# Optimization experiments

Hardware: AMD Instinct MI355X
Metric: run time of the kernel (lower is better)

## Reference

```python
import jax, jax.numpy as jnp
import numpy as np

S, F, H, A, B = 11, 650, 1024, 47, 4096
NEG = -1e9  # stand-in for -inf in masked_fill; softmax weight becomes exactly 0 numerically


def _layernorm(x, g, b):
    m = x.mean(-1, keepdims=True)
    v = ((x - m) ** 2).mean(-1, keepdims=True)
    return (x - m) / jnp.sqrt(v + 1e-5) * g + b


def setup_inputs() -> dict:
    key = jax.random.key(0)
    ks = jax.random.split(key, 16)

    def lin(k, fan_in, fan_out):
        kw, kb = jax.random.split(k)
        s = 1.0 / np.sqrt(fan_in)
        W = jax.random.uniform(kw, (fan_in, fan_out), minval=-s, maxval=s, dtype=jnp.float32)
        b = jax.random.uniform(kb, (fan_out,), minval=-s, maxval=s, dtype=jnp.float32)
        return W, b

    obs = jax.random.normal(ks[0], (B, S, F), dtype=jnp.float32)
    action_mask = jax.random.randint(ks[1], (B, 2, A), 0, 2).astype(jnp.int32)
    action_mask = action_mask.at[:, :, :8].set(1)  # guarantee legal actions per row
    u = jax.random.uniform(ks[2], (B, 2, A), minval=1e-6, maxval=1.0)
    gumbel = -jnp.log(-jnp.log(u))

    W0, b0 = lin(ks[3], S * F, H)
    W1, b1 = lin(ks[4], H, H)
    W2, b2 = lin(ks[5], H, H)
    Wp, bp = lin(ks[6], H, 2 * A)
    Wv, bv = lin(ks[7], H, 1)
    ones = jnp.ones((H,), jnp.float32)
    zeros = jnp.zeros((H,), jnp.float32)
    return {
        'obs': obs, 'action_mask': action_mask, 'gumbel': gumbel,
        'W0': W0, 'b0': b0, 'g0': ones, 'be0': zeros,
        'W1': W1, 'b1': b1, 'g1': ones, 'be1': zeros,
        'W2': W2, 'b2': b2, 'g2': ones, 'be2': zeros,
        'Wp': Wp, 'bp': bp, 'Wv': Wv, 'bv': bv,
    }


def _forward(obs, action_mask, gumbel, W0, b0, g0, be0, W1, b1, g1, be1, W2, b2, g2, be2, Wp, bp, Wv, bv):
    x = obs.reshape(obs.shape[0], -1)
    x = jax.nn.relu(_layernorm(x @ W0 + b0, g0, be0))
    x = jax.nn.relu(_layernorm(x @ W1 + b1, g1, be1))
    x = jax.nn.relu(_layernorm(x @ W2 + b2, g2, be2))  # dropout = eval-mode identity
    policy_logits = (x @ Wp + bp).reshape(-1, 2, A)
    value = (x @ Wv + bv)[:, 0]

    bsz = policy_logits.shape[0]
    rows = jnp.arange(bsz)
    ar = jnp.arange(A)

    # head 1: masked categorical via Gumbel-max
    l1 = jnp.where(action_mask[:, 0, :] == 0, NEG, policy_logits[:, 0, :])
    a1 = jnp.argmax(l1 + gumbel[:, 0, :], axis=-1)
    logp1 = jax.nn.log_softmax(l1, axis=-1)[rows, a1]

    # vectorized mutual-exclusivity mask update (replaces per-batch Python loop)
    m2 = action_mask[:, 1, :]
    oh = ar[None, :] == a1[:, None]
    c_switch = (a1 >= 1) & (a1 <= 6)
    m2 = jnp.where(c_switch[:, None] & oh, 0, m2)
    c_tera = (a1 > 26) & (a1 <= 46)
    rng = (ar >= 27) & (ar < 47)
    m2 = jnp.where(c_tera[:, None] & rng[None, :], 0, m2)
    c_zero = a1 == 0
    col0 = (ar == 0)[None, :]
    m2 = jnp.where(c_zero[:, None] & col0, 0, m2)
    empty = (m2.sum(-1) == 0) & c_zero
    m2 = jnp.where(empty[:, None] & col0, 1, m2)

    l2 = jnp.where(m2 == 0, NEG, policy_logits[:, 1, :])
    a2 = jnp.argmax(l2 + gumbel[:, 1, :], axis=-1)
    logp2 = jax.nn.log_softmax(l2, axis=-1)[rows, a2]

    sampled_actions = jnp.stack([a1, a2], axis=-1)
    policy_log_probs = jnp.stack([logp1, logp2], axis=-1)
    return policy_logits, policy_log_probs, sampled_actions, value


def reference(obs, action_mask, gumbel, W0, b0, g0, be0, W1, b1, g1, be1, W2, b2, g2, be2, Wp, bp, Wv, bv):
    return _forward(obs, action_mask, gumbel, W0, b0, g0, be0, W1, b1, g1, be1, W2, b2, g2, be2, Wp, bp, Wv, bv)
```

## Files before the change

kernel.cpp:

```cpp
#include <hip/hip_runtime.h>
#include <math.h>

#define BATCH 4096
#define HDIM  1024
#define KDIM0 7150
#define KP0   7168
#define KT0   224
#define KTH   32
#define NACT  47
#define NA2   94
#define NEGC  -1000000000.0f

#define LP_OFF  385024
#define ACT_OFF 393216
#define VAL_OFF 401408

typedef _Float16 half8_t  __attribute__((ext_vector_type(8)));
typedef _Float16 half4_t  __attribute__((ext_vector_type(4)));
typedef float    float4_t __attribute__((ext_vector_type(4)));

#define GLOAD16(gp, lp) __builtin_amdgcn_global_load_lds( \
    (__attribute__((address_space(1))) void*)(gp), \
    (__attribute__((address_space(3))) void*)(lp), 16, 0, 0)


__global__ __launch_bounds__(256) void wconv_frag_kernel(
    const float* __restrict__ W, _Float16* __restrict__ Wh,
    _Float16* __restrict__ Wl, int K, int KT)
{
  __shared__ float T[64][65];
  const int k0 = blockIdx.x * 64, n0 = blockIdx.y * 64, t = threadIdx.x;
#pragma unroll
  for (int p = 0; p < 16; ++p) {
    const int idx = p * 256 + t;
    const int r = idx >> 6, c = idx & 63;
    T[r][c] = (k0 + r < K) ? W[(size_t)(k0 + r) * HDIM + n0 + c] : 0.f;
  }
  __syncthreads();
#pragma unroll
  for (int ss = 0; ss < 2; ++ss) {
    const int s    = ss * 256 + t;
    const int tile = s >> 6;
    const int ktl  = tile >> 2, ntl = tile & 3;
    const int lane = s & 63;
    const int quad = lane >> 4, nr = lane & 15;
    half8_t h, l;
#pragma unroll
    for (int j = 0; j < 8; ++j) {
      const float v = T[ktl * 32 + quad * 8 + j][ntl * 16 + nr];
      const _Float16 hh = (_Float16)v;
      h[j] = hh;
      l[j] = (_Float16)((v - (float)hh) * 4096.f);
    }
    const size_t o = ((size_t)((n0 / 16 + ntl) * KT + (k0 / 32 + ktl)) * 64 + lane) * 8;
    *(half8_t*)(Wh + o) = h;
    *(half8_t*)(Wl + o) = l;
  }
}

__global__ __launch_bounds__(256) void adecomp_frag_kernel(
    const float* __restrict__ A, _Float16* __restrict__ Ah,
    _Float16* __restrict__ Al)
{
  __shared__ float Xs[16][257];
  const int t  = threadIdx.x;
  const int mt = blockIdx.y;
  const int kb = blockIdx.x * 256;
  const int lr = t >> 4;
  const int lk = (t & 15) * 16;
  const float* src = A + (size_t)(mt * 16 + lr) * KDIM0 + kb + lk;
#pragma unroll
  for (int c = 0; c < 4; ++c) {
    const int kg = kb + lk + c * 4;
    float4 vv = make_float4(0.f, 0.f, 0.f, 0.f);
    if (kg + 3 < KDIM0) {
      vv = *(const float4*)(src + c * 4);
    } else {
      if (kg     < KDIM0) vv.x = src[c * 4];
      if (kg + 1 < KDIM0) vv.y = src[c * 4 + 1];
      if (kg + 2 < KDIM0) vv.z = src[c * 4 + 2];
      if (kg + 3 < KDIM0) vv.w = src[c * 4 + 3];
    }
    *(float4*)&Xs[lr][lk + c * 4] = vv;
  }
  __syncthreads();
#pragma unroll
  for (int ss = 0; ss < 2; ++ss) {
    const int s    = ss * 256 + t;
    const int ktl  = s >> 6;
    const int lane = s & 63;
    const int quad = lane >> 4, mr = lane & 15;
    half8_t h, l;
#pragma unroll
    for (int j = 0; j < 8; ++j) {
      const float v = Xs[mr][ktl * 32 + quad * 8 + j];
      const _Float16 hh = (_Float16)v;
      h[j] = hh;
      l[j] = (_Float16)((v - (float)hh) * 4096.f);
    }
    const size_t o = ((size_t)(mt * KT0 + blockIdx.x * 8 + ktl) * 64 + lane) * 8;
    *(half8_t*)(Ah + o) = h;
    *(half8_t*)(Al + o) = l;
  }
}

__global__ __launch_bounds__(512, 4) void gemm_frag2_kernel(
    const _Float16* __restrict__ Ah, const _Float16* __restrict__ Al,
    const _Float16* __restrict__ Wh, const _Float16* __restrict__ Wl,
    float* __restrict__ C, int KT, int ktsplit)
{
  __shared__ _Float16 As[2][2][8][512];
  __shared__ _Float16 Ws[2][2][8][512];
  const int t    = threadIdx.x;
  const int lane = t & 63;
  const int w    = t >> 6;
  const int nt0  = blockIdx.x * 8;
  const int mt0  = blockIdx.y * 8;
  const int ktb  = blockIdx.z * ktsplit;
  const int nit  = ktsplit >> 1;
  const int l15  = lane & 15, quad = lane >> 4;
  const int wmi  = (w >> 2) * 4;
  const int wni  = (w & 3) * 2;

  const _Float16* aS[2] = {
    Ah + (size_t)(mt0 + w) * KT * 512 + lane * 8,
    Al + (size_t)(mt0 + w) * KT * 512 + lane * 8 };
  const _Float16* wS[2] = {
    Wh + (size_t)(nt0 + w) * KT * 512 + lane * 8,
    Wl + (size_t)(nt0 + w) * KT * 512 + lane * 8 };

  float4_t acc[4][2], accx[4][2];
#pragma unroll
  for (int i = 0; i < 4; ++i)
#pragma unroll
    for (int j = 0; j < 2; ++j) {
      acc[i][j]  = (float4_t){0.f, 0.f, 0.f, 0.f};
      accx[i][j] = (float4_t){0.f, 0.f, 0.f, 0.f};
    }

  for (int it = 0; it < nit; ++it) {
    const size_t kb = (size_t)(ktb + it * 2) * 512;
#pragma unroll
    for (int k2 = 0; k2 < 2; ++k2)
#pragma unroll
      for (int pl = 0; pl < 2; ++pl) {
        GLOAD16(aS[pl] + kb + k2 * 512, &As[k2][pl][w][0]);
        GLOAD16(wS[pl] + kb + k2 * 512, &Ws[k2][pl][w][0]);
      }
    __syncthreads();
#pragma unroll
    for (int k2 = 0; k2 < 2; ++k2) {
      half8_t ah[4], al[4], wh[2], wl[2];
#pragma unroll
      for (int i = 0; i < 4; ++i) {
        ah[i] = *(const half8_t*)&As[k2][0][wmi + i][lane * 8];
        al[i] = *(const half8_t*)&As[k2][1][wmi + i][lane * 8];
      }
#pragma unroll
      for (int j = 0; j < 2; ++j) {
        wh[j] = *(const half8_t*)&Ws[k2][0][wni + j][lane * 8];
        wl[j] = *(const half8_t*)&Ws[k2][1][wni + j][lane * 8];
      }
#pragma unroll
      for (int i = 0; i < 4; ++i)
#pragma unroll
        for (int j = 0; j < 2; ++j) {
          acc[i][j]  = __builtin_amdgcn_mfma_f32_16x16x32_f16(ah[i], wh[j], acc[i][j], 0, 0, 0);
          accx[i][j] = __builtin_amdgcn_mfma_f32_16x16x32_f16(ah[i], wl[j], accx[i][j], 0, 0, 0);
          accx[i][j] = __builtin_amdgcn_mfma_f32_16x16x32_f16(al[i], wh[j], accx[i][j], 0, 0, 0);
        }
    }
    __syncthreads();
  }

  float* Cb = C + (size_t)blockIdx.z * ((size_t)BATCH * HDIM);
  const float sc = 1.0f / 4096.0f;
#pragma unroll
  for (int i = 0; i < 4; ++i) {
    const int row0 = (mt0 + wmi + i) * 16 + quad * 4;
#pragma unroll
    for (int j = 0; j < 2; ++j) {
      const int col = (nt0 + wni + j) * 16 + l15;
      float* cp = Cb + (size_t)row0 * HDIM + col;
#pragma unroll
      for (int r = 0; r < 4; ++r)
        cp[(size_t)r * HDIM] = acc[i][j][r] + accx[i][j][r] * sc;
    }
  }
}

__global__ __launch_bounds__(1024) void ln_relu_f16_frag_kernel(
    const float* __restrict__ x0, const float* __restrict__ x1,
    const float* __restrict__ bias,
    const float* __restrict__ g, const float* __restrict__ be,
    _Float16* __restrict__ oh, _Float16* __restrict__ ol)
{
  const int t = threadIdx.x;
  const int w = t >> 6, lane = t & 63;
  const int mt = blockIdx.x;
  const float* xr0 = x0 + (size_t)(mt * 16 + w) * HDIM;
  const float* xr1 = x1 + (size_t)(mt * 16 + w) * HDIM;

  float4 v[4];
  float s = 0.f;
#pragma unroll
  for (int c = 0; c < 4; ++c) {
    const int k = c * 256 + lane * 4;
    const float4 a = *(const float4*)(xr0 + k);
    const float4 b = *(const float4*)(xr1 + k);
    const float4 bb = *(const float4*)(bias + k);
    v[c].x = a.x + b.x + bb.x; v[c].y = a.y + b.y + bb.y;
    v[c].z = a.z + b.z + bb.z; v[c].w = a.w + b.w + bb.w;
    s += (v[c].x + v[c].y) + (v[c].z + v[c].w);
  }
#pragma unroll
  for (int o = 32; o; o >>= 1) s += __shfl_xor(s, o, 64);
  const float mean = s * (1.0f / HDIM);

  float s2 = 0.f;
#pragma unroll
  for (int c = 0; c < 4; ++c) {
    v[c].x -= mean; v[c].y -= mean; v[c].z -= mean; v[c].w -= mean;
    s2 += (v[c].x * v[c].x + v[c].y * v[c].y) + (v[c].z * v[c].z + v[c].w * v[c].w);
  }
#pragma unroll
  for (int o = 32; o; o >>= 1) s2 += __shfl_xor(s2, o, 64);
  const float inv = 1.0f / sqrtf(s2 * (1.0f / HDIM) + 1e-5f);

  const int kt_b  = lane >> 3;
  const int quad  = (lane >> 1) & 3;
  const int jb    = (lane & 1) * 4;
#pragma unroll
  for (int c = 0; c < 4; ++c) {
    const int k = c * 256 + lane * 4;
    const float4 gg = *(const float4*)(g + k);
    const float4 ee = *(const float4*)(be + k);
    float r0 = fmaxf(fmaf(v[c].x * inv, gg.x, ee.x), 0.f);
    float r1 = fmaxf(fmaf(v[c].y * inv, gg.y, ee.y), 0.f);
    float r2 = fmaxf(fmaf(v[c].z * inv, gg.z, ee.z), 0.f);
    float r3 = fmaxf(fmaf(v[c].w * inv, gg.w, ee.w), 0.f);
    const _Float16 h0 = (_Float16)r0, h1 = (_Float16)r1, h2 = (_Float16)r2, h3 = (_Float16)r3;
    const half4_t hv = {h0, h1, h2, h3};
    const half4_t lv = {(_Float16)((r0 - (float)h0) * 4096.f),
                        (_Float16)((r1 - (float)h1) * 4096.f),
                        (_Float16)((r2 - (float)h2) * 4096.f),
                        (_Float16)((r3 - (float)h3) * 4096.f)};
    const int kt = c * 8 + kt_b;
    const size_t o = ((size_t)(mt * KTH + kt) * 64 + quad * 16 + w) * 8 + jb;
    *(half4_t*)(oh + o) = hv;
    *(half4_t*)(ol + o) = lv;
  }
}

__global__ __launch_bounds__(256) void pack_wcat_kernel(
    const float* __restrict__ Wp, const float* __restrict__ Wv,
    float* __restrict__ Wc)
{
  const int i = blockIdx.x * 256 + threadIdx.x;
  const int k = i / 96, c = i % 96;
  float v = 0.f;
  if (c < 94)       v = Wp[(size_t)k * 94 + c];
  else if (c == 94) v = Wv[k];
  Wc[i] = v;
}

__global__ __launch_bounds__(256) void head_fused_kernel(
    const float* __restrict__ x0, const float* __restrict__ x1,
    const float* __restrict__ b2, const float* __restrict__ g2,
    const float* __restrict__ be2,
    const float* __restrict__ Wc, const float* __restrict__ bp,
    const float* __restrict__ bv,
    const int* __restrict__ amask, const float* __restrict__ gum,
    float* __restrict__ out)
{
  __shared__ float Xs[8][1025];
  __shared__ float red[4][8][96];
  __shared__ float fl[8][96];
  __shared__ float rstat[16];
  const int t  = threadIdx.x;
  const int r0 = blockIdx.x * 8;
  const int wv = t >> 6, lane = t & 63;

#pragma unroll 4
  for (int i = 0; i < 32; ++i) {
    const int e = i * 256 + t;
    const int r = e >> 10, k = e & 1023;
    const size_t gi = (size_t)(r0 + r) * HDIM + k;
    Xs[r][k] = x0[gi] + x1[gi] + b2[k];
  }
  __syncthreads();

#pragma unroll
  for (int rr = 0; rr < 2; ++rr) {
    const int row = wv + rr * 4;
    float s = 0.f;
#pragma unroll
    for (int ii = 0; ii < 16; ++ii) s += Xs[row][lane + 64 * ii];
#pragma unroll
    for (int o = 32; o; o >>= 1) s += __shfl_xor(s, o, 64);
    const float mean = s * (1.0f / HDIM);
    float s2 = 0.f;
#pragma unroll
    for (int ii = 0; ii < 16; ++ii) {
      const float d = Xs[row][lane + 64 * ii] - mean;
      s2 += d * d;
    }
#pragma unroll
    for (int o = 32; o; o >>= 1) s2 += __shfl_xor(s2, o, 64);
    if (lane == 0) {
      rstat[row] = mean;
      rstat[8 + row] = 1.0f / sqrtf(s2 * (1.0f / HDIM) + 1e-5f);
    }
  }
  __syncthreads();

#pragma unroll 4
  for (int i = 0; i < 32; ++i) {
    const int e = i * 256 + t;
    const int r = e >> 10, k = e & 1023;
    Xs[r][k] = fmaxf(fmaf((Xs[r][k] - rstat[r]) * rstat[8 + r], g2[k], be2[k]), 0.f);
  }
  __syncthreads();

  const int tx = t & 15;
  const int ty = (t >> 4) & 3;
  const int kz = t >> 6;
  const int c0 = tx * 6;
  float acc[2][6] = {{0.f,0.f,0.f,0.f,0.f,0.f},{0.f,0.f,0.f,0.f,0.f,0.f}};
  const int kkend = kz * 256 + 256;
  for (int kk = kz * 256; kk < kkend; ++kk) {
    const float xa = Xs[ty * 2][kk];
    const float xb = Xs[ty * 2 + 1][kk];
    const float* wrow = Wc + (size_t)kk * 96 + c0;
    const float2 w01 = *(const float2*)(wrow);
    const float2 w23 = *(const float2*)(wrow + 2);
    const float2 w45 = *(const float2*)(wrow + 4);
    const float wvv[6] = {w01.x, w01.y, w23.x, w23.y, w45.x, w45.y};
#pragma unroll
    for (int j = 0; j < 6; ++j) {
      acc[0][j] = fmaf(xa, wvv[j], acc[0][j]);
      acc[1][j] = fmaf(xb, wvv[j], acc[1][j]);
    }
  }
#pragma unroll
  for (int r = 0; r < 2; ++r)
#pragma unroll
    for (int j = 0; j < 6; ++j) red[kz][ty * 2 + r][c0 + j] = acc[r][j];
  __syncthreads();

#pragma unroll
  for (int q = 0; q < 3; ++q) {
    const int e = t * 3 + q;
    const int row = e / 96, c = e % 96;
    const float sum = red[0][row][c] + red[1][row][c] + red[2][row][c] + red[3][row][c];
    if (c < 94) {
      const float vv = sum + bp[c];
      out[(size_t)(r0 + row) * NA2 + c] = vv;
      fl[row][c] = vv;
    } else if (c == 94) {
      out[VAL_OFF + r0 + row] = sum + bv[0];
    }
  }
  __syncthreads();

#pragma unroll
  for (int rr = 0; rr < 2; ++rr) {
    const int row = wv + rr * 4;
    const int b = r0 + row;
    const bool valid = lane < NACT;

    const float lg1 = valid ? fl[row][lane] : 0.f;
    const float lg2 = valid ? fl[row][NACT + lane] : 0.f;
    const int   mk1 = valid ? amask[(size_t)b * NA2 + lane] : 0;
    const int   mk2 = valid ? amask[(size_t)b * NA2 + NACT + lane] : 0;
    const float gu1 = valid ? gum[(size_t)b * NA2 + lane] : 0.f;
    const float gu2 = valid ? gum[(size_t)b * NA2 + NACT + lane] : 0.f;

    const float l1 = valid ? ((mk1 == 0) ? NEGC : lg1) : -INFINITY;
    float key = valid ? (l1 + gu1) : -INFINITY;
    int idx = lane;
#pragma unroll
    for (int o = 32; o; o >>= 1) {
      const float ok = __shfl_xor(key, o, 64);
      const int   oi = __shfl_xor(idx, o, 64);
      if (ok > key || (ok == key && oi < idx)) { key = ok; idx = oi; }
    }
    const int a1 = idx;

    float mx = l1;
#pragma unroll
    for (int o = 32; o; o >>= 1) mx = fmaxf(mx, __shfl_xor(mx, o, 64));
    float ex = valid ? expf(l1 - mx) : 0.f;
#pragma unroll
    for (int o = 32; o; o >>= 1) ex += __shfl_xor(ex, o, 64);
    const float logp1 = __shfl(l1, a1, 64) - (mx + logf(ex));

    int m2 = mk2;
    if (a1 >= 1 && a1 <= 6 && lane == a1) m2 = 0;
    if (a1 > 26 && a1 <= 46 && lane >= 27 && valid) m2 = 0;
    if (a1 == 0 && lane == 0) m2 = 0;
    int tot = m2;
#pragma unroll
    for (int o = 32; o; o >>= 1) tot += __shfl_xor(tot, o, 64);
    if (a1 == 0 && tot == 0 && lane == 0) m2 = 1;

    const float l2 = valid ? ((m2 == 0) ? NEGC : lg2) : -INFINITY;
    float key2 = valid ? (l2 + gu2) : -INFINITY;
    int idx2 = lane;
#pragma unroll
    for (int o = 32; o; o >>= 1) {
      const float ok = __shfl_xor(key2, o, 64);
      const int   oi = __shfl_xor(idx2, o, 64);
      if (ok > key2 || (ok == key2 && oi < idx2)) { key2 = ok; idx2 = oi; }
    }
    const int a2 = idx2;

    float mx2 = l2;
#pragma unroll
    for (int o = 32; o; o >>= 1) mx2 = fmaxf(mx2, __shfl_xor(mx2, o, 64));
    float ex2 = valid ? expf(l2 - mx2) : 0.f;
#pragma unroll
    for (int o = 32; o; o >>= 1) ex2 += __shfl_xor(ex2, o, 64);
    const float logp2 = __shfl(l2, a2, 64) - (mx2 + logf(ex2));

    if (lane == 0) {
      out[LP_OFF  + b * 2]     = logp1;
      out[LP_OFF  + b * 2 + 1] = logp2;
      out[ACT_OFF + b * 2]     = (float)a1;
      out[ACT_OFF + b * 2 + 1] = (float)a2;
    }
  }
}

extern "C" void kernel_launch(void* const* d_in, const int* in_sizes, int n_in,
                              void* d_out, int out_size, void* d_ws, size_t ws_size,
                              hipStream_t stream) {
  (void)in_sizes; (void)n_in; (void)out_size; (void)ws_size;
  const float* obs   = (const float*)d_in[0];
  const int*   amask = (const int*)  d_in[1];
  const float* gum   = (const float*)d_in[2];
  const float* W0    = (const float*)d_in[3];
  const float* b0    = (const float*)d_in[4];
  const float* g0    = (const float*)d_in[5];
  const float* be0   = (const float*)d_in[6];
  const float* W1    = (const float*)d_in[7];
  const float* b1    = (const float*)d_in[8];
  const float* g1    = (const float*)d_in[9];
  const float* be1   = (const float*)d_in[10];
  const float* W2    = (const float*)d_in[11];
  const float* b2    = (const float*)d_in[12];
  const float* g2    = (const float*)d_in[13];
  const float* be2   = (const float*)d_in[14];
  const float* Wp    = (const float*)d_in[15];
  const float* bp    = (const float*)d_in[16];
  const float* Wv    = (const float*)d_in[17];
  const float* bv    = (const float*)d_in[18];
  float* out = (float*)d_out;

  char* ws = (char*)d_ws;
  size_t off = 0;
  auto take = [&](size_t n) { char* p = ws + off; off += (n + 255) & ~(size_t)255; return p; };
  _Float16* obsh = (_Float16*)take((size_t)BATCH * KP0 * 2);
  _Float16* obsl = (_Float16*)take((size_t)BATCH * KP0 * 2);
  _Float16* w0h  = (_Float16*)take((size_t)HDIM * KP0 * 2);
  _Float16* w0l  = (_Float16*)take((size_t)HDIM * KP0 * 2);
  _Float16* w1h  = (_Float16*)take((size_t)HDIM * HDIM * 2);
  _Float16* w1l  = (_Float16*)take((size_t)HDIM * HDIM * 2);
  _Float16* w2h  = (_Float16*)take((size_t)HDIM * HDIM * 2);
  _Float16* w2l  = (_Float16*)take((size_t)HDIM * HDIM * 2);
  float*    xf   = (float*)   take((size_t)2 * BATCH * HDIM * 4);
  float*    wc   = (float*)   take((size_t)HDIM * 96 * 4);
  _Float16* xph  = w0h;
  _Float16* xpl  = w0l;
  float* xf1 = xf + (size_t)BATCH * HDIM;

  wconv_frag_kernel<<<dim3(KP0 / 64, 16), 256, 0, stream>>>(W0, w0h, w0l, KDIM0, KT0);
  wconv_frag_kernel<<<dim3(16, 16), 256, 0, stream>>>(W1, w1h, w1l, HDIM, KTH);
  wconv_frag_kernel<<<dim3(16, 16), 256, 0, stream>>>(W2, w2h, w2l, HDIM, KTH);
  pack_wcat_kernel<<<384, 256, 0, stream>>>(Wp, Wv, wc);
  adecomp_frag_kernel<<<dim3(KP0 / 256, BATCH / 16), 256, 0, stream>>>(obs, obsh, obsl);

  gemm_frag2_kernel<<<dim3(8, 32, 2), 512, 0, stream>>>(obsh, obsl, w0h, w0l, xf, KT0, KT0 / 2);
  ln_relu_f16_frag_kernel<<<BATCH / 16, 1024, 0, stream>>>(xf, xf1, b0, g0, be0, xph, xpl);

  gemm_frag2_kernel<<<dim3(8, 32, 2), 512, 0, stream>>>(xph, xpl, w1h, w1l, xf, KTH, KTH / 2);
  ln_relu_f16_frag_kernel<<<BATCH / 16, 1024, 0, stream>>>(xf, xf1, b1, g1, be1, xph, xpl);

  gemm_frag2_kernel<<<dim3(8, 32, 2), 512, 0, stream>>>(xph, xpl, w2h, w2l, xf, KTH, KTH / 2);

  head_fused_kernel<<<BATCH / 8, 256, 0, stream>>>(
      xf, xf1, b2, g2, be2, wc, bp, bv, amask, gum, out);
}
```

Measured before the change: 590.3 us.

## Fuse obs fp16 split-decomposition into first GEMM and remap block order

Removes the separate kernel that split the fp32 observations into high/low fp16 fragment buffers. The first-layer GEMM now reads fp32 obs rows directly, splits them in registers and writes the fragments to shared memory. This avoids writing and re-reading two large fp16 intermediates. Both GEMM kernels also remap block indices so that consecutively launched blocks are spread across M/N tiles, which changes cache locality. The cost is uncoalesced float2 global loads of A done synchronously inside the main loop, instead of async LDS loads.

```diff
diff --git a/kernel.cpp b/kernel.cpp
--- a/kernel.cpp
+++ b/kernel.cpp
@@ -58,49 +58,120 @@
   }
 }
 
-__global__ __launch_bounds__(256) void adecomp_frag_kernel(
-    const float* __restrict__ A, _Float16* __restrict__ Ah,
-    _Float16* __restrict__ Al)
+__global__ __launch_bounds__(512, 4) void gemm_obs_kernel(
+    const float* __restrict__ A,
+    const _Float16* __restrict__ Wh, const _Float16* __restrict__ Wl,
+    float* __restrict__ C, int ktsplit)
 {
-  __shared__ float Xs[16][257];
-  const int t  = threadIdx.x;
-  const int mt = blockIdx.y;
-  const int kb = blockIdx.x * 256;
-  const int lr = t >> 4;
-  const int lk = (t & 15) * 16;
-  const float* src = A + (size_t)(mt * 16 + lr) * KDIM0 + kb + lk;
-#pragma unroll
-  for (int c = 0; c < 4; ++c) {
-    const int kg = kb + lk + c * 4;
-    float4 vv = make_float4(0.f, 0.f, 0.f, 0.f);
-    if (kg + 3 < KDIM0) {
-      vv = *(const float4*)(src + c * 4);
-    } else {
-      if (kg     < KDIM0) vv.x = src[c * 4];
-      if (kg + 1 < KDIM0) vv.y = src[c * 4 + 1];
-      if (kg + 2 < KDIM0) vv.z = src[c * 4 + 2];
-      if (kg + 3 < KDIM0) vv.w = src[c * 4 + 3];
-    }
-    *(float4*)&Xs[lr][lk + c * 4] = vv;
-  }
-  __syncthreads();
-#pragma unroll
-  for (int ss = 0; ss < 2; ++ss) {
-    const int s    = ss * 256 + t;
-    const int ktl  = s >> 6;
-    const int lane = s & 63;
-    const int quad = lane >> 4, mr = lane & 15;
-    half8_t h, l;
-#pragma unroll
-    for (int j = 0; j < 8; ++j) {
-      const float v = Xs[mr][ktl * 32 + quad * 8 + j];
-      const _Float16 hh = (_Float16)v;
-      h[j] = hh;
-      l[j] = (_Float16)((v - (float)hh) * 4096.f);
-    }
-    const size_t o = ((size_t)(mt * KT0 + blockIdx.x * 8 + ktl) * 64 + lane) * 8;
-    *(half8_t*)(Ah + o) = h;
-    *(half8_t*)(Al + o) = l;
+  __shared__ _Float16 As[2][2][8][512];
+  __shared__ _Float16 Ws[2][2][8][512];
+  const int f  = blockIdx.x + 8 * (blockIdx.y + 32 * blockIdx.z);
+  const int nf = (f & 7) * 64 + (f >> 3);
+  const int bx = nf & 7, by = (nf >> 3) & 31, bz = nf >> 8;
+
+  const int t    = threadIdx.x;
+  const int lane = t & 63;
+  const int w    = t >> 6;
+  const int nt0  = bx * 8;
+  const int mt0  = by * 8;
+  const int ktb  = bz * ktsplit;
+  const int nit  = ktsplit >> 1;
+  const int l15  = lane & 15, quad = lane >> 4;
+  const int wmi  = (w >> 2) * 4;
+  const int wni  = (w & 3) * 2;
+
+  const float* aRow = A + (size_t)((mt0 + w) * 16 + l15) * KDIM0 + quad * 8;
+  const _Float16* wS[2] = {
+    Wh + (size_t)(nt0 + w) * KT0 * 512 + lane * 8,
+    Wl + (size_t)(nt0 + w) * KT0 * 512 + lane * 8 };
+
+  float4_t acc[4][2], accx[4][2];
+#pragma unroll
+  for (int i = 0; i < 4; ++i)
+#pragma unroll
+    for (int j = 0; j < 2; ++j) {
+      acc[i][j]  = (float4_t){0.f, 0.f, 0.f, 0.f};
+      accx[i][j] = (float4_t){0.f, 0.f, 0.f, 0.f};
+    }
+
+  for (int it = 0; it < nit; ++it) {
+    const int ktg0 = ktb + it * 2;
+    const size_t kb = (size_t)ktg0 * 512;
+
+    float va[2][8];
+#pragma unroll
+    for (int k2 = 0; k2 < 2; ++k2) {
+      const int kg = (ktg0 + k2) * 32 + quad * 8;
+      const float* src = aRow + (size_t)(ktg0 + k2) * 32;
+      if (kg + 8 <= KDIM0) {
+#pragma unroll
+        for (int c = 0; c < 4; ++c) {
+          const float2 p = *(const float2*)(src + c * 2);
+          va[k2][c * 2] = p.x; va[k2][c * 2 + 1] = p.y;
+        }
+      } else {
+#pragma unroll
+        for (int j = 0; j < 8; ++j)
+          va[k2][j] = (kg + j < KDIM0) ? src[j] : 0.f;
+      }
+    }
+#pragma unroll
+    for (int k2 = 0; k2 < 2; ++k2)
+#pragma unroll
+      for (int pl = 0; pl < 2; ++pl)
+        GLOAD16(wS[pl] + kb + k2 * 512, &Ws[k2][pl][w][0]);
+#pragma unroll
+    for (int k2 = 0; k2 < 2; ++k2) {
+      half8_t h, l;
+#pragma unroll
+      for (int j = 0; j < 8; ++j) {
+        const float v = va[k2][j];
+        const _Float16 hh = (_Float16)v;
+        h[j] = hh;
+        l[j] = (_Float16)((v - (float)hh) * 4096.f);
+      }
+      *(half8_t*)&As[k2][0][w][lane * 8] = h;
+      *(half8_t*)&As[k2][1][w][lane * 8] = l;
+    }
+    __syncthreads();
+#pragma unroll
+    for (int k2 = 0; k2 < 2; ++k2) {
+      half8_t ah[4], al[4], wh[2], wl[2];
+#pragma unroll
+      for (int i = 0; i < 4; ++i) {
+        ah[i] = *(const half8_t*)&As[k2][0][wmi + i][lane * 8];
+        al[i] = *(const half8_t*)&As[k2][1][wmi + i][lane * 8];
+      }
+#pragma unroll
+      for (int j = 0; j < 2; ++j) {
+        wh[j] = *(const half8_t*)&Ws[k2][0][wni + j][lane * 8];
+        wl[j] = *(const half8_t*)&Ws[k2][1][wni + j][lane * 8];
+      }
+#pragma unroll
+      for (int i = 0; i < 4; ++i)
+#pragma unroll
+        for (int j = 0; j < 2; ++j) {
+          acc[i][j]  = __builtin_amdgcn_mfma_f32_16x16x32_f16(ah[i], wh[j], acc[i][j], 0, 0, 0);
+          accx[i][j] = __builtin_amdgcn_mfma_f32_16x16x32_f16(ah[i], wl[j], accx[i][j], 0, 0, 0);
+          accx[i][j] = __builtin_amdgcn_mfma_f32_16x16x32_f16(al[i], wh[j], accx[i][j], 0, 0, 0);
+        }
+    }
+    __syncthreads();
+  }
+
+  float* Cb = C + (size_t)bz * ((size_t)BATCH * HDIM);
+  const float sc = 1.0f / 4096.0f;
+#pragma unroll
+  for (int i = 0; i < 4; ++i) {
+    const int row0 = (mt0 + wmi + i) * 16 + quad * 4;
+#pragma unroll
+    for (int j = 0; j < 2; ++j) {
+      const int col = (nt0 + wni + j) * 16 + l15;
+      float* cp = Cb + (size_t)row0 * HDIM + col;
+#pragma unroll
+      for (int r = 0; r < 4; ++r)
+        cp[(size_t)r * HDIM] = acc[i][j][r] + accx[i][j][r] * sc;
+    }
   }
 }
 
@@ -111,12 +182,16 @@
 {
   __shared__ _Float16 As[2][2][8][512];
   __shared__ _Float16 Ws[2][2][8][512];
+  const int f  = blockIdx.x + 8 * (blockIdx.y + 32 * blockIdx.z);
+  const int nf = (f & 7) * 64 + (f >> 3);
+  const int bx = nf & 7, by = (nf >> 3) & 31, bz = nf >> 8;
+
   const int t    = threadIdx.x;
   const int lane = t & 63;
   const int w    = t >> 6;
-  const int nt0  = blockIdx.x * 8;
-  const int mt0  = blockIdx.y * 8;
-  const int ktb  = blockIdx.z * ktsplit;
+  const int nt0  = bx * 8;
+  const int mt0  = by * 8;
+  const int ktb  = bz * ktsplit;
   const int nit  = ktsplit >> 1;
   const int l15  = lane & 15, quad = lane >> 4;
   const int wmi  = (w >> 2) * 4;
@@ -173,7 +248,7 @@
     __syncthreads();
   }
 
-  float* Cb = C + (size_t)blockIdx.z * ((size_t)BATCH * HDIM);
+  float* Cb = C + (size_t)bz * ((size_t)BATCH * HDIM);
   const float sc = 1.0f / 4096.0f;
 #pragma unroll
   for (int i = 0; i < 4; ++i) {
@@ -460,8 +535,6 @@
   char* ws = (char*)d_ws;
   size_t off = 0;
   auto take = [&](size_t n) { char* p = ws + off; off += (n + 255) & ~(size_t)255; return p; };
-  _Float16* obsh = (_Float16*)take((size_t)BATCH * KP0 * 2);
-  _Float16* obsl = (_Float16*)take((size_t)BATCH * KP0 * 2);
   _Float16* w0h  = (_Float16*)take((size_t)HDIM * KP0 * 2);
   _Float16* w0l  = (_Float16*)take((size_t)HDIM * KP0 * 2);
   _Float16* w1h  = (_Float16*)take((size_t)HDIM * HDIM * 2);
@@ -478,9 +551,8 @@
   wconv_frag_kernel<<<dim3(16, 16), 256, 0, stream>>>(W1, w1h, w1l, HDIM, KTH);
   wconv_frag_kernel<<<dim3(16, 16), 256, 0, stream>>>(W2, w2h, w2l, HDIM, KTH);
   pack_wcat_kernel<<<384, 256, 0, stream>>>(Wp, Wv, wc);
-  adecomp_frag_kernel<<<dim3(KP0 / 256, BATCH / 16), 256, 0, stream>>>(obs, obsh, obsl);
-
-  gemm_frag2_kernel<<<dim3(8, 32, 2), 512, 0, stream>>>(obsh, obsl, w0h, w0l, xf, KT0, KT0 / 2);
+
+  gemm_obs_kernel<<<dim3(8, 32, 2), 512, 0, stream>>>(obs, w0h, w0l, xf, KT0 / 2);
   ln_relu_f16_frag_kernel<<<BATCH / 16, 1024, 0, stream>>>(xf, xf1, b0, g0, be0, xph, xpl);
 
   gemm_frag2_kernel<<<dim3(8, 32, 2), 512, 0, stream>>>(xph, xpl, w1h, w1l, xf, KTH, KTH / 2);
```

Result: faster. 568.6 us (-3.7%).
